# Kernel tuning notes

Measured on AMD Instinct MI355X. Metric: run time of the kernel, lower is better.

The kernel has to match this reference:

```python
import jax, jax.numpy as jnp
import numpy as np

DIM = 2048
MLP_MULT = 4
NUM_EXPERTS = 8
EXPERT_INTER = MLP_MULT * DIM // NUM_EXPERTS  # 1024
B, S = 4, 2048


def setup_inputs() -> dict:
    key = jax.random.key(0)
    k1, k2, k3, k4 = jax.random.split(key, 4)
    x = jax.random.normal(k1, (B, S, DIM), dtype=jnp.float32)
    expert_ids = jax.random.randint(k2, (B, S), 0, NUM_EXPERTS, dtype=jnp.int64)
    # kaiming-uniform-ish scale for gate_up; down_proj random (zeros in orig init
    # would make output trivially zero, unhelpful for a correctness baseline)
    bound_gu = float(np.sqrt(1.0 / DIM))
    gate_up_proj = jax.random.uniform(k3, (NUM_EXPERTS, DIM, 2 * EXPERT_INTER),
                                      dtype=jnp.float32, minval=-bound_gu, maxval=bound_gu)
    bound_dn = float(np.sqrt(1.0 / EXPERT_INTER))
    down_proj = jax.random.uniform(k4, (NUM_EXPERTS, EXPERT_INTER, DIM),
                                   dtype=jnp.float32, minval=-bound_dn, maxval=bound_dn)
    return {"x": x, "expert_ids": expert_ids,
            "gate_up_proj": gate_up_proj, "down_proj": down_proj}


def reference(x, expert_ids, gate_up_proj, down_proj):
    Bb, Ss, D = x.shape
    E = gate_up_proj.shape[0]
    flat_x = x.reshape(-1, D)            # [T, D], T = B*S
    flat_ids = expert_ids.reshape(-1)    # [T]
    # Same math as the torch loop: full dense per-expert MLP, then mask.
    gu = jnp.einsum('td,edh->eth', flat_x, gate_up_proj)       # [E, T, 2I]
    g, u = jnp.split(gu, 2, axis=-1)                           # [E, T, I] each
    h = jax.nn.silu(g) * u                                     # [E, T, I]
    y = jnp.einsum('eti,eid->etd', h, down_proj)               # [E, T, D]
    mask = (flat_ids[None, :] == jnp.arange(E)[:, None])[..., None]  # [E, T, 1]
    out = jnp.sum(y * mask.astype(y.dtype), axis=0)            # [T, D]
    return out.reshape(Bb, Ss, D)
```

## Files before the change

### kernel.cpp

```cpp
#include <hip/hip_runtime.h>
#include <cstdint>
#include <cstddef>


typedef __attribute__((ext_vector_type(8))) _Float16 half8;
typedef __attribute__((ext_vector_type(4))) float floatx4;

#define AS_G __attribute__((address_space(1)))
#define AS_L __attribute__((address_space(3)))

__device__ __forceinline__ void async_cp16(void* lds, const void* g) {
  __builtin_amdgcn_global_load_lds((const AS_G uint32_t*)g, (AS_L uint32_t*)lds,
                                   16, 0, 0);
}

static constexpr int TTOK = 8192;
static constexpr int DIMK = 2048;
static constexpr int EI = 1024;
static constexpr int NE = 8;
static constexpr int PADT = 9216;
static constexpr int MAXTILES = 80;
static constexpr int NTILE_LAUNCH = 72;

__global__ __launch_bounds__(256) void k_route(const int* __restrict__ ids,
                                               int* __restrict__ perm,
                                               int* __restrict__ te,
                                               int* __restrict__ tr0,
                                               int* __restrict__ tnr) {
  __shared__ int cnt[NE];
  __shared__ int cur[NE];
  int tid = threadIdx.x;
  if (tid < NE) cnt[tid] = 0;
  __syncthreads();
  for (int t = tid; t < TTOK; t += 256) atomicAdd(&cnt[ids[t]], 1);
  __syncthreads();
  if (tid == 0) {
    int pr = 0, nt = 0;
    for (int e = 0; e < NE; e++) {
      int n = cnt[e];
      cur[e] = pr;
      for (int j = 0; j < n; j += 128) {
        te[nt] = e; tr0[nt] = pr + j; tnr[nt] = min(128, n - j); nt++;
      }
      pr += ((n + 127) >> 7) << 7;
    }
    for (; nt < MAXTILES; nt++) { te[nt] = 0; tr0[nt] = 0; tnr[nt] = 0; }
  }
  __syncthreads();
  for (int i = tid; i < PADT; i += 256) perm[i] = 0;
  __syncthreads();
  for (int t = tid; t < TTOK; t += 256) {
    int p = atomicAdd(&cur[ids[t]], 1);
    perm[p] = t;
  }
}

__global__ __launch_bounds__(256) void k_gather_cvt(
    const float* __restrict__ x, const int* __restrict__ perm,
    _Float16* __restrict__ xg) {
  int r = blockIdx.x;
  int tok = perm[r];
  int c = threadIdx.x * 8;
  const float* s = x + (size_t)tok * DIMK + c;
  float4 a = *(const float4*)s;
  float4 b = *(const float4*)(s + 4);
  half8 o;
  o[0] = (_Float16)a.x; o[1] = (_Float16)a.y;
  o[2] = (_Float16)a.z; o[3] = (_Float16)a.w;
  o[4] = (_Float16)b.x; o[5] = (_Float16)b.y;
  o[6] = (_Float16)b.z; o[7] = (_Float16)b.w;
  *(half8*)(xg + (size_t)r * DIMK + c) = o;
}

template <int K, int N>
__global__ __launch_bounds__(256) void k_transpose_cvt(
    const float* __restrict__ src, _Float16* __restrict__ dst) {
  __shared__ float tile[64][67];
  int e = blockIdx.z;
  int n0 = blockIdx.x * 64, k0 = blockIdx.y * 64;
  const float* s = src + (size_t)e * K * N;
  _Float16* d = dst + (size_t)e * N * K;
  int tid = threadIdx.x;
  int kk = tid >> 4;
  int nn = (tid & 15) * 4;
#pragma unroll
  for (int i = 0; i < 4; i++) {
    float4 v = *(const float4*)(s + (size_t)(k0 + kk + i * 16) * N + n0 + nn);
    tile[kk + i * 16][nn + 0] = v.x;
    tile[kk + i * 16][nn + 1] = v.y;
    tile[kk + i * 16][nn + 2] = v.z;
    tile[kk + i * 16][nn + 3] = v.w;
  }
  __syncthreads();
  int nrow = tid >> 3;
  int k8 = (tid & 7) * 8;
#pragma unroll
  for (int i = 0; i < 2; i++) {
    int n = nrow + i * 32;
    half8 o;
#pragma unroll
    for (int j = 0; j < 8; j++) o[j] = (_Float16)tile[k8 + j][n];
    *(half8*)(d + (size_t)(n0 + n) * K + k0 + k8) = o;
  }
}

__global__ __launch_bounds__(256) void k_gateup(
    const _Float16* __restrict__ xg, const _Float16* __restrict__ wt1,
    const int* __restrict__ te, const int* __restrict__ tr0,
    const int* __restrict__ tnr, _Float16* __restrict__ hbuf) {
  int tile = blockIdx.y;
  int nr = tnr[tile];
  if (nr == 0) return;
  int e = te[tile], r0 = tr0[tile];
  int col = blockIdx.x * 64;
  int tid = threadIdx.x;

  __shared__ __align__(16) _Float16 As[128 * 32];
  __shared__ __align__(16) _Float16 Bg[64 * 32];
  __shared__ __align__(16) _Float16 Bu[64 * 32];

  int an = tid >> 2;
  int aq = (tid & 3) ^ ((tid >> 3) & 3);
  const _Float16* ap0 = xg + (size_t)(r0 + an) * DIMK + aq * 8;
  const _Float16* ap1 = xg + (size_t)(r0 + 64 + an) * DIMK + aq * 8;
  _Float16* al0 = As + (size_t)tid * 8;
  _Float16* al1 = As + 2048 + (size_t)tid * 8;

  int bn = tid >> 2;
  int bq = (tid & 3) ^ ((tid >> 3) & 3);
  const _Float16* bgp =
      wt1 + (size_t)e * DIMK * DIMK + (size_t)(col + bn) * DIMK + bq * 8;
  const _Float16* bup = bgp + (size_t)EI * DIMK;
  _Float16* bgl = Bg + (size_t)tid * 8;
  _Float16* bul = Bu + (size_t)tid * 8;

  int wave = tid >> 6, lane = tid & 63;
  int wm = (wave & 1) * 64, wn = (wave >> 1) * 32;
  int lm = lane & 15, lq = lane >> 4;
  int aoff[4], boff[2];
#pragma unroll
  for (int i = 0; i < 4; i++) {
    int r = wm + i * 16 + lm;
    aoff[i] = (r * 4 + (lq ^ ((r >> 1) & 3))) * 8;
  }
#pragma unroll
  for (int j = 0; j < 2; j++) {
    int n = wn + j * 16 + lm;
    boff[j] = (n * 4 + (lq ^ ((n >> 1) & 3))) * 8;
  }

  floatx4 accg[4][2], accu[4][2];
#pragma unroll
  for (int i = 0; i < 4; i++)
#pragma unroll
    for (int j = 0; j < 2; j++) {
      accg[i][j] = (floatx4)0.0f;
      accu[i][j] = (floatx4)0.0f;
    }

  for (int k0 = 0; k0 < DIMK; k0 += 32) {
    async_cp16(al0, ap0 + k0);
    async_cp16(al1, ap1 + k0);
    async_cp16(bgl, bgp + k0);
    async_cp16(bul, bup + k0);
    __syncthreads();
    half8 af[4], bgf[2], buf_[2];
#pragma unroll
    for (int i = 0; i < 4; i++) af[i] = *(const half8*)(As + aoff[i]);
#pragma unroll
    for (int j = 0; j < 2; j++) {
      bgf[j] = *(const half8*)(Bg + boff[j]);
      buf_[j] = *(const half8*)(Bu + boff[j]);
    }
#pragma unroll
    for (int i = 0; i < 4; i++)
#pragma unroll
      for (int j = 0; j < 2; j++) {
        accg[i][j] = __builtin_amdgcn_mfma_f32_16x16x32_f16(af[i], bgf[j],
                                                            accg[i][j], 0, 0, 0);
        accu[i][j] = __builtin_amdgcn_mfma_f32_16x16x32_f16(af[i], buf_[j],
                                                            accu[i][j], 0, 0, 0);
      }
    __syncthreads();
  }

#pragma unroll
  for (int i = 0; i < 4; i++) {
    int rbase = wm + i * 16 + lq * 4;
#pragma unroll
    for (int j = 0; j < 2; j++) {
      int c = col + wn + j * 16 + lm;
#pragma unroll
      for (int rr = 0; rr < 4; rr++) {
        float g = accg[i][j][rr];
        float u = accu[i][j][rr];
        float h = g / (1.0f + __expf(-g)) * u;
        hbuf[(size_t)(r0 + rbase + rr) * EI + c] = (_Float16)h;
      }
    }
  }
}

__global__ __launch_bounds__(256) void k_down(
    const _Float16* __restrict__ hbuf, const _Float16* __restrict__ wt2,
    const int* __restrict__ perm, const int* __restrict__ te,
    const int* __restrict__ tr0, const int* __restrict__ tnr,
    float* __restrict__ out) {
  int tile = blockIdx.y;
  int nr = tnr[tile];
  if (nr == 0) return;
  int e = te[tile], r0 = tr0[tile];
  int col = blockIdx.x * 128;
  int tid = threadIdx.x;

  __shared__ __align__(16) _Float16 As[128 * 32];
  __shared__ __align__(16) _Float16 Bs[128 * 32];

  int an = tid >> 2;
  int aq = (tid & 3) ^ ((tid >> 3) & 3);
  const _Float16* ap0 = hbuf + (size_t)(r0 + an) * EI + aq * 8;
  const _Float16* ap1 = hbuf + (size_t)(r0 + 64 + an) * EI + aq * 8;
  _Float16* al0 = As + (size_t)tid * 8;
  _Float16* al1 = As + 2048 + (size_t)tid * 8;
  const _Float16* wte = wt2 + (size_t)e * DIMK * EI;
  const _Float16* bp0 = wte + (size_t)(col + an) * EI + aq * 8;
  const _Float16* bp1 = wte + (size_t)(col + 64 + an) * EI + aq * 8;
  _Float16* bl0 = Bs + (size_t)tid * 8;
  _Float16* bl1 = Bs + 2048 + (size_t)tid * 8;

  int wave = tid >> 6, lane = tid & 63;
  int wm = (wave & 1) * 64, wn = (wave >> 1) * 64;
  int lm = lane & 15, lq = lane >> 4;
  int aoff[4], boff[4];
#pragma unroll
  for (int i = 0; i < 4; i++) {
    int r = wm + i * 16 + lm;
    aoff[i] = (r * 4 + (lq ^ ((r >> 1) & 3))) * 8;
    int n = wn + i * 16 + lm;
    boff[i] = (n * 4 + (lq ^ ((n >> 1) & 3))) * 8;
  }

  floatx4 acc[4][4];
#pragma unroll
  for (int i = 0; i < 4; i++)
#pragma unroll
    for (int j = 0; j < 4; j++) acc[i][j] = (floatx4)0.0f;

  for (int k0 = 0; k0 < EI; k0 += 32) {
    async_cp16(al0, ap0 + k0);
    async_cp16(al1, ap1 + k0);
    async_cp16(bl0, bp0 + k0);
    async_cp16(bl1, bp1 + k0);
    __syncthreads();
    half8 af[4], bf[4];
#pragma unroll
    for (int i = 0; i < 4; i++) {
      af[i] = *(const half8*)(As + aoff[i]);
      bf[i] = *(const half8*)(Bs + boff[i]);
    }
#pragma unroll
    for (int i = 0; i < 4; i++)
#pragma unroll
      for (int j = 0; j < 4; j++)
        acc[i][j] =
            __builtin_amdgcn_mfma_f32_16x16x32_f16(af[i], bf[j], acc[i][j], 0, 0, 0);
    __syncthreads();
  }

#pragma unroll
  for (int i = 0; i < 4; i++) {
    int rbase = wm + i * 16 + lq * 4;
#pragma unroll
    for (int rr = 0; rr < 4; rr++) {
      int r = rbase + rr;
      if (r < nr) {
        int tok = perm[r0 + r];
        float* orow = out + (size_t)tok * DIMK + col;
#pragma unroll
        for (int j = 0; j < 4; j++) orow[wn + j * 16 + lm] = acc[i][j][rr];
      }
    }
  }
}

extern "C" void kernel_launch(void* const* d_in, const int* in_sizes, int n_in,
                              void* d_out, int out_size, void* d_ws,
                              size_t ws_size, hipStream_t stream) {
  const float* x = (const float*)d_in[0];
  const int* ids = (const int*)d_in[1];
  const float* gup = (const float*)d_in[2];
  const float* dwn = (const float*)d_in[3];
  float* out = (float*)d_out;
  char* ws = (char*)d_ws;

  int* perm = (int*)ws;
  int* te = (int*)(ws + 36864);
  int* tr0 = (int*)(ws + 36864 + 512);
  int* tnr = (int*)(ws + 36864 + 1024);
  _Float16* wt1 = (_Float16*)(ws + 65536);
  _Float16* hbuf = (_Float16*)(ws + 65536 + 67108864);
  _Float16* xg = (_Float16*)(ws + 65536 + 67108864 + 18874368);
  _Float16* wt2 = wt1;

  k_route<<<dim3(1), dim3(256), 0, stream>>>(ids, perm, te, tr0, tnr);
  k_gather_cvt<<<dim3(PADT), dim3(256), 0, stream>>>(x, perm, xg);
  k_transpose_cvt<2048, 2048>
      <<<dim3(32, 32, 8), dim3(256), 0, stream>>>(gup, wt1);
  k_gateup<<<dim3(16, NTILE_LAUNCH), dim3(256), 0, stream>>>(
      xg, wt1, te, tr0, tnr, hbuf);
  k_transpose_cvt<1024, 2048>
      <<<dim3(32, 16, 8), dim3(256), 0, stream>>>(dwn, wt2);
  k_down<<<dim3(16, NTILE_LAUNCH), dim3(256), 0, stream>>>(
      hbuf, wt2, perm, te, tr0, tnr, out);
}
```

Baseline: 520.3 us.

## Parallelize routing scatter, fuse gather with weight transpose, widen GEMM K-step

After: 491.5 us. -5.5%, faster.

```diff
diff --git a/kernel.cpp b/kernel.cpp
--- a/kernel.cpp
+++ b/kernel.cpp
@@ -26,9 +26,12 @@
                                                int* __restrict__ perm,
                                                int* __restrict__ te,
                                                int* __restrict__ tr0,
-                                               int* __restrict__ tnr) {
+                                               int* __restrict__ tnr,
+                                               int* __restrict__ cur) {
   __shared__ int cnt[NE];
-  __shared__ int cur[NE];
+  __shared__ int sstart[NE];
+  __shared__ int snpad[NE];
+  __shared__ int stotal;
   int tid = threadIdx.x;
   if (tid < NE) cnt[tid] = 0;
   __syncthreads();
@@ -38,49 +41,50 @@
     int pr = 0, nt = 0;
     for (int e = 0; e < NE; e++) {
       int n = cnt[e];
+      sstart[e] = pr;
       cur[e] = pr;
+      int padded = ((n + 127) >> 7) << 7;
+      snpad[e] = padded - n;
       for (int j = 0; j < n; j += 128) {
         te[nt] = e; tr0[nt] = pr + j; tnr[nt] = min(128, n - j); nt++;
       }
-      pr += ((n + 127) >> 7) << 7;
-    }
+      pr += padded;
+    }
+    stotal = pr;
     for (; nt < MAXTILES; nt++) { te[nt] = 0; tr0[nt] = 0; tnr[nt] = 0; }
   }
   __syncthreads();
-  for (int i = tid; i < PADT; i += 256) perm[i] = 0;
-  __syncthreads();
-  for (int t = tid; t < TTOK; t += 256) {
-    int p = atomicAdd(&cur[ids[t]], 1);
-    perm[p] = t;
-  }
-}
-
-__global__ __launch_bounds__(256) void k_gather_cvt(
-    const float* __restrict__ x, const int* __restrict__ perm,
-    _Float16* __restrict__ xg) {
-  int r = blockIdx.x;
-  int tok = perm[r];
-  int c = threadIdx.x * 8;
-  const float* s = x + (size_t)tok * DIMK + c;
-  float4 a = *(const float4*)s;
-  float4 b = *(const float4*)(s + 4);
-  half8 o;
-  o[0] = (_Float16)a.x; o[1] = (_Float16)a.y;
-  o[2] = (_Float16)a.z; o[3] = (_Float16)a.w;
-  o[4] = (_Float16)b.x; o[5] = (_Float16)b.y;
-  o[6] = (_Float16)b.z; o[7] = (_Float16)b.w;
-  *(half8*)(xg + (size_t)r * DIMK + c) = o;
+  for (int e = 0; e < NE; e++) {
+    int base = sstart[e] + cnt[e];
+    for (int i = tid; i < snpad[e]; i += 256) perm[base + i] = 0;
+  }
+  for (int i = stotal + tid; i < PADT; i += 256) perm[i] = 0;
+}
+
+__global__ __launch_bounds__(256) void k_scatter(const int* __restrict__ ids,
+                                                 int* __restrict__ cur,
+                                                 int* __restrict__ perm) {
+  __shared__ int bcnt[NE], bbase[NE], bloc[NE];
+  int tid = threadIdx.x;
+  int t = blockIdx.x * 256 + tid;
+  if (tid < NE) { bcnt[tid] = 0; bloc[tid] = 0; }
+  __syncthreads();
+  int e = ids[t];
+  atomicAdd(&bcnt[e], 1);
+  __syncthreads();
+  if (tid < NE && bcnt[tid] > 0) bbase[tid] = atomicAdd(&cur[tid], bcnt[tid]);
+  __syncthreads();
+  int off = atomicAdd(&bloc[e], 1);
+  perm[bbase[e] + off] = t;
 }
 
 template <int K, int N>
-__global__ __launch_bounds__(256) void k_transpose_cvt(
-    const float* __restrict__ src, _Float16* __restrict__ dst) {
-  __shared__ float tile[64][67];
-  int e = blockIdx.z;
-  int n0 = blockIdx.x * 64, k0 = blockIdx.y * 64;
+__device__ __forceinline__ void transpose_tile(const float* __restrict__ src,
+                                               _Float16* __restrict__ dst,
+                                               float (*tile)[67], int e,
+                                               int n0, int k0, int tid) {
   const float* s = src + (size_t)e * K * N;
   _Float16* d = dst + (size_t)e * N * K;
-  int tid = threadIdx.x;
   int kk = tid >> 4;
   int nn = (tid & 15) * 4;
 #pragma unroll
@@ -102,6 +106,42 @@
     for (int j = 0; j < 8; j++) o[j] = (_Float16)tile[k8 + j][n];
     *(half8*)(d + (size_t)(n0 + n) * K + k0 + k8) = o;
   }
+}
+
+__global__ __launch_bounds__(256) void k_prep(const float* __restrict__ gup,
+                                              _Float16* __restrict__ wt1,
+                                              const float* __restrict__ x,
+                                              const int* __restrict__ perm,
+                                              _Float16* __restrict__ xg) {
+  __shared__ float tile[64][67];
+  int b = blockIdx.x;
+  int tid = threadIdx.x;
+  if (b < 8192) {
+    int e = b >> 10;
+    int r = b & 1023;
+    transpose_tile<DIMK, DIMK>(gup, wt1, tile, e, (r & 31) * 64, (r >> 5) * 64,
+                               tid);
+  } else {
+    int row = b - 8192;
+    int tok = perm[row];
+    int c = tid * 8;
+    const float* s = x + (size_t)tok * DIMK + c;
+    float4 a = *(const float4*)s;
+    float4 bb = *(const float4*)(s + 4);
+    half8 o;
+    o[0] = (_Float16)a.x; o[1] = (_Float16)a.y;
+    o[2] = (_Float16)a.z; o[3] = (_Float16)a.w;
+    o[4] = (_Float16)bb.x; o[5] = (_Float16)bb.y;
+    o[6] = (_Float16)bb.z; o[7] = (_Float16)bb.w;
+    *(half8*)(xg + (size_t)row * DIMK + c) = o;
+  }
+}
+
+__global__ __launch_bounds__(256) void k_t2(const float* __restrict__ dwn,
+                                            _Float16* __restrict__ wt2) {
+  __shared__ float tile[64][67];
+  transpose_tile<EI, DIMK>(dwn, wt2, tile, blockIdx.z, blockIdx.x * 64,
+                           blockIdx.y * 64, threadIdx.x);
 }
 
 __global__ __launch_bounds__(256) void k_gateup(
@@ -115,21 +155,18 @@
   int col = blockIdx.x * 64;
   int tid = threadIdx.x;
 
-  __shared__ __align__(16) _Float16 As[128 * 32];
-  __shared__ __align__(16) _Float16 Bg[64 * 32];
-  __shared__ __align__(16) _Float16 Bu[64 * 32];
+  __shared__ __align__(16) _Float16 As[128 * 64];
+  __shared__ __align__(16) _Float16 Bg[64 * 64];
+  __shared__ __align__(16) _Float16 Bu[64 * 64];
 
   int an = tid >> 2;
   int aq = (tid & 3) ^ ((tid >> 3) & 3);
   const _Float16* ap0 = xg + (size_t)(r0 + an) * DIMK + aq * 8;
-  const _Float16* ap1 = xg + (size_t)(r0 + 64 + an) * DIMK + aq * 8;
+  const _Float16* ap1 = ap0 + (size_t)64 * DIMK;
   _Float16* al0 = As + (size_t)tid * 8;
   _Float16* al1 = As + 2048 + (size_t)tid * 8;
-
-  int bn = tid >> 2;
-  int bq = (tid & 3) ^ ((tid >> 3) & 3);
   const _Float16* bgp =
-      wt1 + (size_t)e * DIMK * DIMK + (size_t)(col + bn) * DIMK + bq * 8;
+      wt1 + (size_t)e * DIMK * DIMK + (size_t)(col + an) * DIMK + aq * 8;
   const _Float16* bup = bgp + (size_t)EI * DIMK;
   _Float16* bgl = Bg + (size_t)tid * 8;
   _Float16* bul = Bu + (size_t)tid * 8;
@@ -158,29 +195,39 @@
       accu[i][j] = (floatx4)0.0f;
     }
 
-  for (int k0 = 0; k0 < DIMK; k0 += 32) {
+  for (int k0 = 0; k0 < DIMK; k0 += 64) {
     async_cp16(al0, ap0 + k0);
     async_cp16(al1, ap1 + k0);
     async_cp16(bgl, bgp + k0);
     async_cp16(bul, bup + k0);
+    async_cp16(al0 + 4096, ap0 + k0 + 32);
+    async_cp16(al1 + 4096, ap1 + k0 + 32);
+    async_cp16(bgl + 2048, bgp + k0 + 32);
+    async_cp16(bul + 2048, bup + k0 + 32);
     __syncthreads();
-    half8 af[4], bgf[2], buf_[2];
-#pragma unroll
-    for (int i = 0; i < 4; i++) af[i] = *(const half8*)(As + aoff[i]);
-#pragma unroll
-    for (int j = 0; j < 2; j++) {
-      bgf[j] = *(const half8*)(Bg + boff[j]);
-      buf_[j] = *(const half8*)(Bu + boff[j]);
-    }
-#pragma unroll
-    for (int i = 0; i < 4; i++)
+#pragma unroll
+    for (int s = 0; s < 2; s++) {
+      const _Float16* Ab = As + s * 4096;
+      const _Float16* Bgb = Bg + s * 2048;
+      const _Float16* Bub = Bu + s * 2048;
+      half8 af[4], bgf[2], buf_[2];
+#pragma unroll
+      for (int i = 0; i < 4; i++) af[i] = *(const half8*)(Ab + aoff[i]);
 #pragma unroll
       for (int j = 0; j < 2; j++) {
-        accg[i][j] = __builtin_amdgcn_mfma_f32_16x16x32_f16(af[i], bgf[j],
-                                                            accg[i][j], 0, 0, 0);
-        accu[i][j] = __builtin_amdgcn_mfma_f32_16x16x32_f16(af[i], buf_[j],
-                                                            accu[i][j], 0, 0, 0);
-      }
+        bgf[j] = *(const half8*)(Bgb + boff[j]);
+        buf_[j] = *(const half8*)(Bub + boff[j]);
+      }
+#pragma unroll
+      for (int i = 0; i < 4; i++)
+#pragma unroll
+        for (int j = 0; j < 2; j++) {
+          accg[i][j] = __builtin_amdgcn_mfma_f32_16x16x32_f16(
+              af[i], bgf[j], accg[i][j], 0, 0, 0);
+          accu[i][j] = __builtin_amdgcn_mfma_f32_16x16x32_f16(
+              af[i], buf_[j], accu[i][j], 0, 0, 0);
+        }
+    }
     __syncthreads();
   }
 
@@ -213,18 +260,18 @@
   int col = blockIdx.x * 128;
   int tid = threadIdx.x;
 
-  __shared__ __align__(16) _Float16 As[128 * 32];
-  __shared__ __align__(16) _Float16 Bs[128 * 32];
+  __shared__ __align__(16) _Float16 As[128 * 64];
+  __shared__ __align__(16) _Float16 Bs[128 * 64];
 
   int an = tid >> 2;
   int aq = (tid & 3) ^ ((tid >> 3) & 3);
   const _Float16* ap0 = hbuf + (size_t)(r0 + an) * EI + aq * 8;
-  const _Float16* ap1 = hbuf + (size_t)(r0 + 64 + an) * EI + aq * 8;
+  const _Float16* ap1 = ap0 + (size_t)64 * EI;
   _Float16* al0 = As + (size_t)tid * 8;
   _Float16* al1 = As + 2048 + (size_t)tid * 8;
   const _Float16* wte = wt2 + (size_t)e * DIMK * EI;
   const _Float16* bp0 = wte + (size_t)(col + an) * EI + aq * 8;
-  const _Float16* bp1 = wte + (size_t)(col + 64 + an) * EI + aq * 8;
+  const _Float16* bp1 = bp0 + (size_t)64 * EI;
   _Float16* bl0 = Bs + (size_t)tid * 8;
   _Float16* bl1 = Bs + 2048 + (size_t)tid * 8;
 
@@ -246,24 +293,33 @@
 #pragma unroll
     for (int j = 0; j < 4; j++) acc[i][j] = (floatx4)0.0f;
 
-  for (int k0 = 0; k0 < EI; k0 += 32) {
+  for (int k0 = 0; k0 < EI; k0 += 64) {
     async_cp16(al0, ap0 + k0);
     async_cp16(al1, ap1 + k0);
     async_cp16(bl0, bp0 + k0);
     async_cp16(bl1, bp1 + k0);
+    async_cp16(al0 + 4096, ap0 + k0 + 32);
+    async_cp16(al1 + 4096, ap1 + k0 + 32);
+    async_cp16(bl0 + 4096, bp0 + k0 + 32);
+    async_cp16(bl1 + 4096, bp1 + k0 + 32);
     __syncthreads();
-    half8 af[4], bf[4];
-#pragma unroll
-    for (int i = 0; i < 4; i++) {
-      af[i] = *(const half8*)(As + aoff[i]);
-      bf[i] = *(const half8*)(Bs + boff[i]);
-    }
-#pragma unroll
-    for (int i = 0; i < 4; i++)
-#pragma unroll
-      for (int j = 0; j < 4; j++)
-        acc[i][j] =
-            __builtin_amdgcn_mfma_f32_16x16x32_f16(af[i], bf[j], acc[i][j], 0, 0, 0);
+#pragma unroll
+    for (int s = 0; s < 2; s++) {
+      const _Float16* Ab = As + s * 4096;
+      const _Float16* Bb = Bs + s * 4096;
+      half8 af[4], bf[4];
+#pragma unroll
+      for (int i = 0; i < 4; i++) {
+        af[i] = *(const half8*)(Ab + aoff[i]);
+        bf[i] = *(const half8*)(Bb + boff[i]);
+      }
+#pragma unroll
+      for (int i = 0; i < 4; i++)
+#pragma unroll
+        for (int j = 0; j < 4; j++)
+          acc[i][j] = __builtin_amdgcn_mfma_f32_16x16x32_f16(af[i], bf[j],
+                                                             acc[i][j], 0, 0, 0);
+    }
     __syncthreads();
   }
 
@@ -297,19 +353,18 @@
   int* te = (int*)(ws + 36864);
   int* tr0 = (int*)(ws + 36864 + 512);
   int* tnr = (int*)(ws + 36864 + 1024);
+  int* cur = (int*)(ws + 36864 + 1536);
   _Float16* wt1 = (_Float16*)(ws + 65536);
   _Float16* hbuf = (_Float16*)(ws + 65536 + 67108864);
   _Float16* xg = (_Float16*)(ws + 65536 + 67108864 + 18874368);
   _Float16* wt2 = wt1;
 
-  k_route<<<dim3(1), dim3(256), 0, stream>>>(ids, perm, te, tr0, tnr);
-  k_gather_cvt<<<dim3(PADT), dim3(256), 0, stream>>>(x, perm, xg);
-  k_transpose_cvt<2048, 2048>
-      <<<dim3(32, 32, 8), dim3(256), 0, stream>>>(gup, wt1);
+  k_route<<<dim3(1), dim3(256), 0, stream>>>(ids, perm, te, tr0, tnr, cur);
+  k_scatter<<<dim3(32), dim3(256), 0, stream>>>(ids, cur, perm);
+  k_prep<<<dim3(8192 + PADT), dim3(256), 0, stream>>>(gup, wt1, x, perm, xg);
   k_gateup<<<dim3(16, NTILE_LAUNCH), dim3(256), 0, stream>>>(
       xg, wt1, te, tr0, tnr, hbuf);
-  k_transpose_cvt<1024, 2048>
-      <<<dim3(32, 16, 8), dim3(256), 0, stream>>>(dwn, wt2);
+  k_t2<<<dim3(32, 16, 8), dim3(256), 0, stream>>>(dwn, wt2);
   k_down<<<dim3(16, NTILE_LAUNCH), dim3(256), 0, stream>>>(
       hbuf, wt2, perm, te, tr0, tnr, out);
 }
```
